# Kernel optimization log

Measured on AMD Instinct MI355X. Metric: run time of the kernel, lower is better.

The kernel has to match this reference:

```python
import jax, jax.numpy as jnp
import numpy as np

N_ATOMS = 10000
N_STRUCT = 100
N_PSEUDO = 4
N_SPECIES = 4
NMAX = 8
LMAX = 3
HIDDEN = 256
Q = NMAX * N_PSEUDO            # 32 radial*pseudo channels per l
N_FEAT = (LMAX + 1) * Q * Q    # 4096


def setup_inputs() -> dict:
    key = jax.random.key(0)
    ks = jax.random.split(key, 12)
    inp = {}
    for l in range(LMAX + 1):
        inp[f"c{l}"] = jax.random.normal(ks[l], (N_ATOMS, 2 * l + 1, Q), dtype=jnp.float32)
    inp["species_idx"] = jax.random.randint(ks[4], (N_ATOMS,), 0, N_SPECIES, dtype=jnp.int32)
    inp["structure_ids"] = jnp.sort(jax.random.randint(ks[5], (N_ATOMS,), 0, N_STRUCT, dtype=jnp.int32))
    inp["comb_W"] = jax.random.normal(ks[6], (N_PSEUDO, N_SPECIES), dtype=jnp.float32) / np.sqrt(N_SPECIES).astype(np.float32)
    inp["W0"] = jax.random.normal(ks[7], (N_PSEUDO, N_FEAT, HIDDEN), dtype=jnp.float32) / np.sqrt(N_FEAT).astype(np.float32)
    inp["W1"] = jax.random.normal(ks[8], (N_PSEUDO, HIDDEN, HIDDEN), dtype=jnp.float32) / np.sqrt(HIDDEN).astype(np.float32)
    inp["W2"] = jax.random.normal(ks[9], (N_PSEUDO, HIDDEN, 1), dtype=jnp.float32) / np.sqrt(HIDDEN).astype(np.float32)
    return inp


def _power_spectrum(cs):
    # Per-atom outer-product contraction over m, per angular order l.
    feats = []
    for l, c in enumerate(cs):  # c: [A, 2l+1, Q]
        cg = np.float32(1.0 / np.sqrt(2 * l + 1))
        ps = cg * jnp.einsum('amq,amr->aqr', c, c)  # [A, Q, Q]
        feats.append(ps.reshape(c.shape[0], -1))
    return jnp.concatenate(feats, axis=-1)  # [A, N_FEAT]


def reference(c0, c1, c2, c3, species_idx, structure_ids, comb_W, W0, W1, W2):
    features = _power_spectrum([c0, c1, c2, c3])  # [A, F]
    # species-gathered pseudo-species weights: one_hot(a_i) @ combination_matrix
    one_hot = jax.nn.one_hot(species_idx, N_SPECIES, dtype=features.dtype)  # [A, S]
    pw = one_hot @ comb_W.T  # [A, P]
    # embedded_features = features[:, :, None] * pw[:, None, :]
    emb = features[:, None, :] * pw[:, :, None]  # [A, P, F]
    # distinct no-bias MLP per pseudo species (SiLU activations)
    h = jax.nn.silu(jnp.einsum('apf,pfh->aph', emb, W0))
    h = jax.nn.silu(jnp.einsum('aph,phg->apg', h, W1))
    atomic = jnp.einsum('apg,pgo->apo', h, W2)[..., 0].sum(axis=1)  # [A]
    # scatter-sum atomic energies into per-structure totals (index_add_)
    energies = jax.ops.segment_sum(atomic, structure_ids, num_segments=N_STRUCT)
    return energies.reshape(-1, 1)
```

## Files before the change

### kernel.cpp

```cpp
#include <hip/hip_runtime.h>
#include <hip/hip_bf16.h>
#include <cstdint>
#include <cstddef>

#define N_ATOMS 10000
#define NSTRUCT 100
#define NP 4
#define NS 4
#define NF2 2560
#define HID 256
#define APAD 10240

#define PB_FEAT  2500
#define PB_W0    (PB_FEAT + 2560)
#define PB_W1    (PB_W0 + 256)
#define PB_ZERO  (PB_W1 + 300)
#define PB_TOTAL (PB_ZERO + 1)

typedef __attribute__((ext_vector_type(8))) _Float16 f16x8;
typedef __attribute__((ext_vector_type(8))) ushort u16x8;
typedef __attribute__((ext_vector_type(4))) float f32x4;

__device__ __forceinline__ float silu(float x) {
  return x / (1.f + __expf(-x));
}
__device__ __forceinline__ ushort f2h(float x) {
  _Float16 h = (_Float16)x;
  return *reinterpret_cast<ushort*>(&h);
}
__device__ __forceinline__ void cdec(int c, int& q, int& b) {
  if (c < 32)      { q = c >> 2; b = c & 3; }
  else if (c < 56) { int x = c - 32; int j = (x * 171) >> 9; q = 8 + j; b = 1 + (x - j * 3); }
  else if (c < 72) { int x = c - 56; q = 16 + (x >> 1); b = 2 + (x & 1); }
  else             { q = 24 + (c - 72); b = 3; }
}

typedef __attribute__((address_space(3))) uint32_t lds_u32;
typedef __attribute__((address_space(3))) ushort lds_ushort;
typedef const __attribute__((address_space(1))) uint32_t glb_u32;
__device__ __forceinline__ void glds16(const ushort* g, ushort* l) {
  __builtin_amdgcn_global_load_lds((glb_u32*)g, (lds_u32*)l, 16, 0, 0);
}
__device__ __forceinline__ f16x8 dsr(uint32_t addr) {
  f16x8 r;
  asm volatile("ds_read_b128 %0, %1" : "=v"(r) : "v"(addr));
  return r;
}

__global__ __launch_bounds__(256) void prep_kernel(
    const float* __restrict__ c0, const float* __restrict__ c1,
    const float* __restrict__ c2, const float* __restrict__ c3,
    const float* __restrict__ W0, const float* __restrict__ W1,
    ushort* __restrict__ fh, ushort* __restrict__ W0t,
    ushort* __restrict__ W1t, float* __restrict__ out) {
  __shared__ float shbuf[2048];
  int b = blockIdx.x;
  int tid = threadIdx.x;

  if (b < PB_FEAT) {
    int wv = tid >> 6, lane = tid & 63;
    int a = b * 4 + wv;
    float* cs = shbuf + wv * 512;
    for (int i = 0; i < 8; ++i) {
      int e = lane + i * 64;
      float v;
      if (e < 32)       v = c0[a * 32  + e];
      else if (e < 128) v = c1[a * 96  + (e - 32)];
      else if (e < 288) v = c2[a * 160 + (e - 128)];
      else              v = c3[a * 224 + (e - 288)];
      cs[e] = v;
    }
    __syncthreads();
    const float cg[4]  = {1.0f, 0.5773502691896258f, 0.4472135954999579f, 0.3779644730092272f};
    const int  off[4]  = {0, 32, 128, 288};
    const int  nm[4]   = {1, 3, 5, 7};
#pragma unroll
    for (int t = 0; t < 5; ++t) {
      int cc = lane + t * 64;
      int l = cc / 80, c = cc - l * 80;
      int q, bb; cdec(c, q, bb);
      int rb = bb * 8;
      const float* base = cs + off[l];
      float s[8] = {0.f, 0.f, 0.f, 0.f, 0.f, 0.f, 0.f, 0.f};
      for (int m = 0; m < nm[l]; ++m) {
        float bq = base[m * 32 + q];
        float4 v0 = *reinterpret_cast<const float4*>(&base[m * 32 + rb]);
        float4 v1 = *reinterpret_cast<const float4*>(&base[m * 32 + rb + 4]);
        s[0] += bq * v0.x; s[1] += bq * v0.y; s[2] += bq * v0.z; s[3] += bq * v0.w;
        s[4] += bq * v1.x; s[5] += bq * v1.y; s[6] += bq * v1.z; s[7] += bq * v1.w;
      }
      u16x8 o;
#pragma unroll
      for (int u = 0; u < 8; ++u) o[u] = f2h(s[u] * cg[l]);
      *reinterpret_cast<u16x8*>(&fh[(size_t)a * NF2 + cc * 8]) = o;
    }
  } else if (b < PB_W0) {
    int idx = b - PB_FEAT;
    int nx = idx & 7;
    int rest = idx >> 3;
    int ky = rest % 80, p = rest / 80;
    int kt = ky * 32, nt = nx * 32;
    int lx = tid & 31, ly = tid >> 5;
    float (*t)[33] = (float(*)[33])shbuf;
    const float* src = W0 + (size_t)p * 4096 * HID;
#pragma unroll
    for (int i = 0; i < 4; ++i) {
      int kf = kt + ly + i * 8;
      int l = kf / 640, w = kf - l * 640;
      int c = w >> 3, s = w & 7;
      int q, bb; cdec(c, q, bb);
      int r = bb * 8 + s;
      float v = 0.f;
      if (r >= q) {
        v = src[(size_t)(l * 1024 + q * 32 + r) * HID + nt + lx];
        if (r > q) v += src[(size_t)(l * 1024 + r * 32 + q) * HID + nt + lx];
      }
      t[ly + i * 8][lx] = v;
    }
    __syncthreads();
    ushort* dst = W0t + (size_t)p * HID * NF2;
#pragma unroll
    for (int i = 0; i < 4; ++i)
      dst[(size_t)(nt + ly + i * 8) * NF2 + kt + lx] = f2h(t[lx][ly + i * 8]);
  } else if (b < PB_W1) {
    int idx = b - PB_W0;
    int nx = idx & 7, ky = (idx >> 3) & 7, p = idx >> 6;
    int kt = ky * 32, nt = nx * 32;
    int lx = tid & 31, ly = tid >> 5;
    float (*t)[33] = (float(*)[33])shbuf;
    const float* src = W1 + (size_t)p * HID * HID;
#pragma unroll
    for (int i = 0; i < 4; ++i)
      t[ly + i * 8][lx] = src[(size_t)(kt + ly + i * 8) * HID + nt + lx];
    __syncthreads();
    ushort* dst = W1t + (size_t)p * HID * HID;
#pragma unroll
    for (int i = 0; i < 4; ++i)
      dst[(size_t)(nt + ly + i * 8) * HID + kt + lx] = f2h(t[lx][ly + i * 8]);
  } else if (b < PB_ZERO) {
    int idx = b - PB_W1;
    size_t e = (size_t)idx * 2048 + tid * 8;
    u16x8 z = (u16x8){0, 0, 0, 0, 0, 0, 0, 0};
    *reinterpret_cast<u16x8*>(&fh[(size_t)N_ATOMS * NF2 + e]) = z;
  } else {
    if (tid < NSTRUCT) out[tid] = 0.f;
  }
}

__global__ __launch_bounds__(256) void gemm0_mfma(
    const ushort* __restrict__ fh, const ushort* __restrict__ W0t,
    const float* __restrict__ combW, const int* __restrict__ species,
    ushort* __restrict__ h0f) {
  __shared__ ushort sh[16384];
  int tid = threadIdx.x;
  int linear = blockIdx.y * 8 + blockIdx.x;
  int xc = linear & 7, sq = linear >> 3;
  int bm = ((sq >> 3) * 8 + xc) * 128;
  int bn = (sq & 7) * 128;
  int wid = tid >> 6, lane = tid & 63;
  int wm = (wid >> 1) * 64, wn = (wid & 1) * 64;
  int mh = wid >> 1, nh = wid & 1;

  int pr = tid >> 3, pc = tid & 7;
  int lg = pc ^ (pr & 7);
  int mhalf = lg >> 2, kc = lg & 3;
  const ushort* gA1 = fh  + ((size_t)(bm + pr + 64 * mhalf) * NF2 + kc * 8);
  const ushort* gA2 = gA1 + (size_t)32 * NF2;
  const ushort* gB1 = W0t + ((size_t)(bn + pr + 64 * mhalf) * NF2 + kc * 8);
  const ushort* gB2 = gB1 + (size_t)32 * NF2;
  ushort* l0 = sh + tid * 8;

#define STAGE(B) do {                          \
    glds16(gA1, l0 + (B) * 8192);              \
    glds16(gA2, l0 + (B) * 8192 + 2048);       \
    glds16(gB1, l0 + (B) * 8192 + 4096);       \
    glds16(gB2, l0 + (B) * 8192 + 6144);       \
    gA1 += 32; gA2 += 32; gB1 += 32; gB2 += 32; } while (0)

  f32x4 acc[4][4];
#pragma unroll
  for (int i = 0; i < 4; ++i)
#pragma unroll
    for (int j = 0; j < 4; ++j) acc[i][j] = (f32x4){0.f, 0.f, 0.f, 0.f};

  int mrow = lane & 15, qv = lane >> 4, h7 = mrow & 7;
  int pcA = ((mh << 2) | qv) ^ h7;
  int pcB = ((nh << 2) | qv) ^ h7;
  uint32_t lbase = (uint32_t)(size_t)(lds_ushort*)sh;
  uint32_t aA[4], aB[4];
#pragma unroll
  for (int i = 0; i < 4; ++i) {
    aA[i] = lbase + 2u * (uint32_t)((i * 16 + mrow) * 64 + pcA * 8);
    aB[i] = lbase + 2u * (uint32_t)(4096 + (i * 16 + mrow) * 64 + pcB * 8);
  }

  STAGE(0);
  STAGE(1);
  asm volatile("s_waitcnt vmcnt(4)" ::: "memory");
  __builtin_amdgcn_s_barrier();

  const int NK = NF2 / 32;
  for (int t = 0; t < NK; ++t) {
    uint32_t bb = (uint32_t)(t & 1) * 16384u;
    f16x8 af[4], bf[4];
#pragma unroll
    for (int i = 0; i < 4; ++i) {
      af[i] = dsr(aA[i] + bb);
      bf[i] = dsr(aB[i] + bb);
    }
    asm volatile("s_waitcnt lgkmcnt(0)" ::: "memory");
    __builtin_amdgcn_sched_barrier(0);
#pragma unroll
    for (int i = 0; i < 4; ++i)
#pragma unroll
      for (int j = 0; j < 4; ++j)
        acc[i][j] = __builtin_amdgcn_mfma_f32_16x16x32_f16(af[i], bf[j], acc[i][j], 0, 0, 0);
    __builtin_amdgcn_s_barrier();
    if (t < NK - 2) {
      STAGE(t & 1);
      asm volatile("s_waitcnt vmcnt(4)" ::: "memory");
    } else {
      asm volatile("s_waitcnt vmcnt(0)" ::: "memory");
    }
    __builtin_amdgcn_s_barrier();
  }
#undef STAGE

  int p = bn >> 8;
  int col = lane & 15, rbase = (lane >> 4) * 4;
#pragma unroll
  for (int i = 0; i < 4; ++i) {
#pragma unroll
    for (int r = 0; r < 4; ++r) {
      int m = bm + wm + i * 16 + rbase + r;
      bool live = (m < N_ATOMS);
      float pw = live ? combW[p * NS + species[m]] : 0.f;
#pragma unroll
      for (int j = 0; j < 4; ++j) {
        int n = bn + wn + j * 16 + col;
        float v = live ? silu(pw * acc[i][j][r]) : 0.f;
        h0f[(size_t)m * 1024 + n] = f2h(v);
      }
    }
  }
}

__global__ __launch_bounds__(256) void mlp1_mfma(
    const ushort* __restrict__ h0f, const ushort* __restrict__ W1t,
    const float* __restrict__ W2, const int* __restrict__ sid,
    float* __restrict__ out) {
  __shared__ ushort As[64 * 256];
  __shared__ float sout[NSTRUCT];
  int tid = threadIdx.x;
  int linear = blockIdx.x;
  int xc = linear & 7, s = linear >> 3;
  int p = s & 3, t = s >> 2;
  int bm = ((t >> 1) * 8 + xc) * 128 + (t & 1) * 64;
  int wid = tid >> 6, lane = tid & 63;
  int wn = wid * 64;

  if (tid < NSTRUCT) sout[tid] = 0.f;

  int mrow = lane & 15;
  int qv = lane >> 4;
  int h7 = mrow & 7;

#pragma unroll
  for (int s8 = 0; s8 < 8; ++s8) {
    int d = s8 * 256 + tid;
    int r = d >> 5, pcs = d & 31;
    int lc = pcs ^ (r & 7);
    glds16(h0f + (size_t)(bm + r) * 1024 + p * 256 + lc * 8, As + d * 8);
  }

  const ushort* wb = W1t + (size_t)p * HID * HID;
  f16x8 breg[4][8];
#pragma unroll
  for (int j = 0; j < 4; ++j) {
    const ushort* row = wb + (size_t)(wn + j * 16 + mrow) * 256 + qv * 8;
#pragma unroll
    for (int ki = 0; ki < 8; ++ki)
      breg[j][ki] = *reinterpret_cast<const f16x8*>(row + ki * 32);
  }

  __syncthreads();

  f32x4 acc[4][4];
#pragma unroll
  for (int i = 0; i < 4; ++i)
#pragma unroll
    for (int j = 0; j < 4; ++j) acc[i][j] = (f32x4){0.f, 0.f, 0.f, 0.f};

#pragma unroll
  for (int ki = 0; ki < 8; ++ki) {
    f16x8 af[4];
#pragma unroll
    for (int i = 0; i < 4; ++i) {
      int row = i * 16 + mrow;
      int pc2 = (ki * 4 + qv) ^ h7;
      af[i] = *reinterpret_cast<const f16x8*>(&As[row * 256 + pc2 * 8]);
    }
#pragma unroll
    for (int i = 0; i < 4; ++i)
#pragma unroll
      for (int j = 0; j < 4; ++j)
        acc[i][j] = __builtin_amdgcn_mfma_f32_16x16x32_f16(af[i], breg[j][ki], acc[i][j], 0, 0, 0);
  }

  int col = lane & 15, quad = lane >> 4;
  float w2j[4];
#pragma unroll
  for (int j = 0; j < 4; ++j) w2j[j] = W2[p * 256 + wn + j * 16 + col];
#pragma unroll
  for (int i = 0; i < 4; ++i) {
#pragma unroll
    for (int r = 0; r < 4; ++r) {
      float v = silu(acc[i][0][r]) * w2j[0] + silu(acc[i][1][r]) * w2j[1]
              + silu(acc[i][2][r]) * w2j[2] + silu(acc[i][3][r]) * w2j[3];
      v += __shfl_xor(v, 1, 64);
      v += __shfl_xor(v, 2, 64);
      v += __shfl_xor(v, 4, 64);
      v += __shfl_xor(v, 8, 64);
      if (col == 0) {
        int m = bm + i * 16 + quad * 4 + r;
        if (m < N_ATOMS) atomicAdd(&sout[sid[m]], v);
      }
    }
  }
  __syncthreads();
  if (tid < NSTRUCT) {
    float v = sout[tid];
    if (v != 0.f) atomicAdd(&out[tid], v);
  }
}

extern "C" void kernel_launch(void* const* d_in, const int* in_sizes, int n_in,
                              void* d_out, int out_size, void* d_ws, size_t ws_size,
                              hipStream_t stream) {
  const float* c0      = (const float*)d_in[0];
  const float* c1      = (const float*)d_in[1];
  const float* c2      = (const float*)d_in[2];
  const float* c3      = (const float*)d_in[3];
  const int*   species = (const int*)d_in[4];
  const int*   sid     = (const int*)d_in[5];
  const float* combW   = (const float*)d_in[6];
  const float* W0      = (const float*)d_in[7];
  const float* W1      = (const float*)d_in[8];
  const float* W2      = (const float*)d_in[9];
  float*       out     = (float*)d_out;

  ushort* fh  = (ushort*)d_ws;
  ushort* W0t = fh  + (size_t)APAD * NF2;
  ushort* W1t = W0t + (size_t)NP * HID * NF2;
  ushort* h0f = W1t + (size_t)NP * HID * HID;

  prep_kernel<<<PB_TOTAL, 256, 0, stream>>>(c0, c1, c2, c3, W0, W1,
                                            fh, W0t, W1t, out);

  dim3 g2(8, APAD / 128);
  gemm0_mfma<<<g2, 256, 0, stream>>>(fh, W0t, combW, species, h0f);

  mlp1_mfma<<<640, 256, 0, stream>>>(h0f, W1t, W2, sid, out);
}
```

Baseline: 210.0 us.

## Use triple-buffered LDS in gemm0 with one barrier per K step

The GEMM0 main loop moves from a double-buffered LDS ring with two barriers per iteration to a three-slot ring. Each iteration issues the next global-to-LDS stage before the fragment reads and MFMAs, and uses a single barrier. The goal is to overlap loads with compute and halve barrier stalls. The cost is 48 KB of LDS per block instead of 32 KB, which may reduce occupancy, and the vmcnt accounting becomes more delicate.

After: 215.7 us. 2.7% more time.

```diff
diff --git a/kernel.cpp b/kernel.cpp
--- a/kernel.cpp
+++ b/kernel.cpp
@@ -151,7 +151,7 @@
     const ushort* __restrict__ fh, const ushort* __restrict__ W0t,
     const float* __restrict__ combW, const int* __restrict__ species,
     ushort* __restrict__ h0f) {
-  __shared__ ushort sh[16384];
+  __shared__ ushort sh[24576];
   int tid = threadIdx.x;
   int linear = blockIdx.y * 8 + blockIdx.x;
   int xc = linear & 7, sq = linear >> 3;
@@ -170,11 +170,11 @@
   const ushort* gB2 = gB1 + (size_t)32 * NF2;
   ushort* l0 = sh + tid * 8;
 
-#define STAGE(B) do {                          \
-    glds16(gA1, l0 + (B) * 8192);              \
-    glds16(gA2, l0 + (B) * 8192 + 2048);       \
-    glds16(gB1, l0 + (B) * 8192 + 4096);       \
-    glds16(gB2, l0 + (B) * 8192 + 6144);       \
+#define STAGE(OFF) do {                        \
+    glds16(gA1, l0 + (OFF));                   \
+    glds16(gA2, l0 + (OFF) + 2048);            \
+    glds16(gB1, l0 + (OFF) + 4096);            \
+    glds16(gB2, l0 + (OFF) + 6144);            \
     gA1 += 32; gA2 += 32; gB1 += 32; gB2 += 32; } while (0)
 
   f32x4 acc[4][4];
@@ -195,18 +195,23 @@
   }
 
   STAGE(0);
-  STAGE(1);
+  STAGE(8192);
   asm volatile("s_waitcnt vmcnt(4)" ::: "memory");
   __builtin_amdgcn_s_barrier();
 
   const int NK = NF2 / 32;
+  int stoff = 16384;
+  uint32_t rboff = 0;
   for (int t = 0; t < NK; ++t) {
-    uint32_t bb = (uint32_t)(t & 1) * 16384u;
+    if (t + 2 < NK) {
+      STAGE(stoff);
+      stoff += 8192; if (stoff == 24576) stoff = 0;
+    }
     f16x8 af[4], bf[4];
 #pragma unroll
     for (int i = 0; i < 4; ++i) {
-      af[i] = dsr(aA[i] + bb);
-      bf[i] = dsr(aB[i] + bb);
+      af[i] = dsr(aA[i] + rboff);
+      bf[i] = dsr(aB[i] + rboff);
     }
     asm volatile("s_waitcnt lgkmcnt(0)" ::: "memory");
     __builtin_amdgcn_sched_barrier(0);
@@ -215,14 +220,13 @@
 #pragma unroll
       for (int j = 0; j < 4; ++j)
         acc[i][j] = __builtin_amdgcn_mfma_f32_16x16x32_f16(af[i], bf[j], acc[i][j], 0, 0, 0);
-    __builtin_amdgcn_s_barrier();
-    if (t < NK - 2) {
-      STAGE(t & 1);
+    if (t + 2 < NK) {
       asm volatile("s_waitcnt vmcnt(4)" ::: "memory");
-    } else {
+    } else if (t + 1 < NK) {
       asm volatile("s_waitcnt vmcnt(0)" ::: "memory");
     }
-    __builtin_amdgcn_s_barrier();
+    if (t + 1 < NK) __builtin_amdgcn_s_barrier();
+    rboff += 16384; if (rboff == 49152) rboff = 0;
   }
 #undef STAGE
 
```
